# Kernel tuning notes

Measured on AMD Instinct MI355X. Metric: run time of the kernel, lower is better.

## Reference

```python
import jax, jax.numpy as jnp
import numpy as np

VOCAB = 50000
D = 300          # w2v vector_size
B = 2048         # sentences
L = 64           # maxlen
S = 2048         # total seeds (= sum of num_clusters[0])
C = 64           # clusters
LS = 8           # maxlen_seed
ANPHA = 0.5


def setup_inputs() -> dict:
    key = jax.random.key(0)
    ks = jax.random.split(key, 4)
    return {
        "sents": jax.random.randint(ks[0], (B, L), 0, VOCAB),
        "seeds": jax.random.randint(ks[1], (S, LS), 0, VOCAB),
        "num_clusters": jnp.full((1, C), S // C, dtype=jnp.int32),
        "num_arr": 0,
        "mask": jnp.ones((B, L), jnp.float32),
        "flag": 1,
        "emb_teacher": jax.random.normal(ks[2], (VOCAB, D), jnp.float32) * 0.1,
        "emb_student": jax.random.normal(ks[3], (VOCAB, D), jnp.float32) * 0.1,
    }


def _sent_emb(tok_emb, mask):
    # masked mean pooling over tokens: tok_emb [B,L,D], mask [B,L]
    denom = jnp.clip(mask.sum(-1, keepdims=True), 1.0)
    return (tok_emb * mask[..., None]).sum(1) / denom


def _seed_emb(tok_emb):
    # plain mean pooling over seed-phrase tokens: [S,LS,D] -> [S,D]
    return tok_emb.mean(1)


def _segment_max_arg(pro, lens):
    # pro [B,S]; lens [C] segment lengths summing to S (ragged segments along axis 1)
    Ssz = pro.shape[1]
    Csz = lens.shape[0]
    csum = jnp.cumsum(lens)
    starts = csum - lens
    seg = jnp.searchsorted(csum, jnp.arange(Ssz), side="right")   # [S] segment ids
    m = jax.ops.segment_max(pro.T, seg, num_segments=Csz)          # [C,B] per-segment max
    is_max = pro.T == m[seg]                                       # [S,B]
    local = jnp.arange(Ssz) - starts[seg]                          # index within segment
    arg = jax.ops.segment_min(jnp.where(is_max, local[:, None], Ssz), seg,
                              num_segments=Csz)                    # first argmax (torch tie rule)
    return m.T, arg.T                                              # [B,C], [B,C]


def _normalize(x):
    # Normalize(): class-probabilities + reliability (confidence vs uniform)
    p = jax.nn.softmax(x, axis=-1)
    reli = jnp.max(p, axis=-1, keepdims=True) - 1.0 / x.shape[-1]
    return p, reli


def reference(sents, seeds, num_clusters, num_arr, mask, flag,
              emb_teacher, emb_student):
    lens = num_clusters[0]

    # teacher branch
    snt_t = _sent_emb(emb_teacher[sents], mask)        # [B,D]
    sd_t = _seed_emb(emb_teacher[seeds])               # [S,D]
    pro_t = jnp.einsum("bd,sd->bs", snt_t, sd_t)       # [B,S]

    # student branch
    snt_s = _sent_emb(emb_student[sents], mask)
    sd_s = _seed_emb(emb_student[seeds])
    pro_s = jnp.einsum("bd,sd->bs", snt_s, sd_s)

    # ragged per-cluster max / argmax (replaces the torch loop + cat)
    pro_s_max, index_max = _segment_max_arg(pro_s, lens)   # [B,C]
    pro_t_max, _ = _segment_max_arg(pro_t, lens)           # [B,C]

    predict_t, reli_t = _normalize(pro_t_max)

    if flag:  # flag is a static python int -> loss branch
        denta = predict_t - pro_s_max
        loss = ((1.0 + ANPHA * jnp.abs(reli_t)) * denta * denta).sum()
        return loss / predict_t.shape[0]
    else:
        return jnp.argmax(pro_s_max, axis=-1)
```

## Files before the change

kernel.cpp:

```cpp
#include <hip/hip_runtime.h>
#include <hip/hip_bf16.h>

#define BB 2048
#define LL 64
#define SS 2048
#define LSEED 8
#define CC 64
#define DD 300
#define NC4 75
#define KP 320

typedef __attribute__((ext_vector_type(8))) short short8;
typedef __attribute__((ext_vector_type(4))) float f32x4;

__device__ __forceinline__ unsigned enc_f(float f) {
    unsigned u = __float_as_uint(f);
    return (u & 0x80000000u) ? ~u : (u | 0x80000000u);
}
__device__ __forceinline__ float dec_f(unsigned k) {
    unsigned u = (k & 0x80000000u) ? (k ^ 0x80000000u) : ~k;
    return __uint_as_float(u);
}
__device__ __forceinline__ unsigned short f2bf(float f) {
    unsigned u = __float_as_uint(f);
    u += 0x7fffu + ((u >> 16) & 1u);
    return (unsigned short)(u >> 16);
}
__device__ __forceinline__ void gload_lds16(const void* g, void* l) {
    __builtin_amdgcn_global_load_lds(
        (const __attribute__((address_space(1))) void*)g,
        (__attribute__((address_space(3))) void*)l, 16, 0, 0);
}

__global__ __launch_bounds__(256) void pool_kernel(
    const int* __restrict__ sents, const int* __restrict__ seeds,
    const int* __restrict__ lens, const float* __restrict__ mask,
    const float* __restrict__ emb_t, const float* __restrict__ emb_s,
    unsigned short* __restrict__ snt_t, unsigned short* __restrict__ snt_s,
    unsigned short* __restrict__ sd_t, unsigned short* __restrict__ sd_s,
    unsigned* __restrict__ keys_all, int* __restrict__ seg,
    float* __restrict__ out0) {
    const int bid = blockIdx.x, tid = threadIdx.x;

    if (tid < 64) keys_all[bid * 64 + tid] = 0u;
    if (bid == 0) {
        if (tid == 0) *out0 = 0.f;
        for (int i = tid * 8; i < tid * 8 + 8; i++) {
            int c = 0, cum = lens[0];
            while (i >= cum && c < CC - 1) { c++; cum += lens[c]; }
            seg[i] = c;
        }
    }

    __shared__ float4 pt[3 * NC4];
    __shared__ float4 ps[3 * NC4];
    __shared__ int toks[LL];
    __shared__ float msk[LL];
    __shared__ float denom_sh;

    const int g = tid / NC4;
    const int c = tid - g * NC4;

    if (bid < BB) {
        const int b = bid;
        if (tid < LL) {
            float v = mask[b * LL + tid];
            msk[tid] = v;
            toks[tid] = sents[b * LL + tid];
#pragma unroll
            for (int d = 32; d; d >>= 1) v += __shfl_xor(v, d);
            if (tid == 0) denom_sh = fmaxf(v, 1.0f);
        }
        __syncthreads();
        if (g < 3) {
            float4 at = {0.f, 0.f, 0.f, 0.f}, as = {0.f, 0.f, 0.f, 0.f};
#pragma unroll 4
            for (int l = g; l < LL; l += 3) {
                size_t o = (size_t)toks[l] * DD;
                float m = msk[l];
                float4 vt = *(const float4*)(emb_t + o + 4 * c);
                float4 vs = *(const float4*)(emb_s + o + 4 * c);
                at.x = fmaf(m, vt.x, at.x); at.y = fmaf(m, vt.y, at.y);
                at.z = fmaf(m, vt.z, at.z); at.w = fmaf(m, vt.w, at.w);
                as.x = fmaf(m, vs.x, as.x); as.y = fmaf(m, vs.y, as.y);
                as.z = fmaf(m, vs.z, as.z); as.w = fmaf(m, vs.w, as.w);
            }
            pt[g * NC4 + c] = at;
            ps[g * NC4 + c] = as;
        }
        __syncthreads();
        float scale = 1.0f / denom_sh;
        if (tid < 150) {
            int table = tid / NC4, cc = tid - table * NC4;
            const float4* P = table ? ps : pt;
            float4 a = P[cc], b2 = P[NC4 + cc], d2 = P[2 * NC4 + cc];
            ushort4 o;
            o.x = f2bf((a.x + b2.x + d2.x) * scale);
            o.y = f2bf((a.y + b2.y + d2.y) * scale);
            o.z = f2bf((a.z + b2.z + d2.z) * scale);
            o.w = f2bf((a.w + b2.w + d2.w) * scale);
            unsigned short* dst = (table ? snt_s : snt_t) + (size_t)b * KP + 4 * cc;
            *(ushort4*)dst = o;
        } else if (tid >= 160 && tid < 170) {
            int k = tid - 160;
            unsigned short* dst = ((k < 5) ? snt_t : snt_s) + (size_t)b * KP + 300 + 4 * (k % 5);
            *(ushort4*)dst = (ushort4){0, 0, 0, 0};
        }
    } else {
        const int s = bid - BB;
        if (tid < LSEED) toks[tid] = seeds[s * LSEED + tid];
        __syncthreads();
        if (g < 3) {
            float4 at = {0.f, 0.f, 0.f, 0.f}, as = {0.f, 0.f, 0.f, 0.f};
#pragma unroll
            for (int l = g; l < LSEED; l += 3) {
                size_t o = (size_t)toks[l] * DD;
                float4 vt = *(const float4*)(emb_t + o + 4 * c);
                float4 vs = *(const float4*)(emb_s + o + 4 * c);
                at.x += vt.x; at.y += vt.y; at.z += vt.z; at.w += vt.w;
                as.x += vs.x; as.y += vs.y; as.z += vs.z; as.w += vs.w;
            }
            pt[g * NC4 + c] = at;
            ps[g * NC4 + c] = as;
        }
        __syncthreads();
        const float scale = 1.0f / LSEED;
        if (tid < 150) {
            int table = tid / NC4, cc = tid - table * NC4;
            const float4* P = table ? ps : pt;
            float4 a = P[cc], b2 = P[NC4 + cc], d2 = P[2 * NC4 + cc];
            ushort4 o;
            o.x = f2bf((a.x + b2.x + d2.x) * scale);
            o.y = f2bf((a.y + b2.y + d2.y) * scale);
            o.z = f2bf((a.z + b2.z + d2.z) * scale);
            o.w = f2bf((a.w + b2.w + d2.w) * scale);
            unsigned short* dst = (table ? sd_s : sd_t) + (size_t)s * KP + 4 * cc;
            *(ushort4*)dst = o;
        } else if (tid >= 160 && tid < 170) {
            int k = tid - 160;
            unsigned short* dst = ((k < 5) ? sd_t : sd_s) + (size_t)s * KP + 300 + 4 * (k % 5);
            *(ushort4*)dst = (ushort4){0, 0, 0, 0};
        }
    }
}

__global__ __launch_bounds__(256) void gemm_max_kernel(
    const unsigned short* __restrict__ snt_t, const unsigned short* __restrict__ snt_s,
    const unsigned short* __restrict__ sd_t, const unsigned short* __restrict__ sd_s,
    const int* __restrict__ seg,
    unsigned* __restrict__ keys_t, unsigned* __restrict__ keys_s) {
    const int branch = blockIdx.z;
    const unsigned short* Ag = branch ? snt_s : snt_t;
    const unsigned short* Bg = branch ? sd_s : sd_t;
    unsigned* keys = branch ? keys_s : keys_t;

    const int tid = threadIdx.x;
    const int wave = tid >> 6, lane = tid & 63;
    const int quad = lane >> 4, l16 = lane & 15;
    const int wm = wave >> 1, wn = wave & 1;
    const int row0 = blockIdx.y * 128, col0 = blockIdx.x * 128;

    __shared__ __align__(16) char smem[33792 + 512];
    unsigned short* As = (unsigned short*)smem;
    unsigned short* Bs = As + 128 * 32;
    float* Dl = (float*)smem;
    int* segs = (int*)(smem + 33792);

    if (tid < 128) segs[tid] = seg[col0 + tid];

    const int lr = lane >> 2, lp = lane & 3;

    f32x4 acc[4][4];
#pragma unroll
    for (int i = 0; i < 4; i++)
#pragma unroll
        for (int j = 0; j < 4; j++) acc[i][j] = (f32x4)0.f;

#pragma unroll 1
    for (int kt = 0; kt < KP / 32; kt++) {
        const int k0 = kt * 32;
        __syncthreads();
#pragma unroll
        for (int i = 0; i < 2; i++) {
            int rb = wave * 32 + i * 16;
            gload_lds16(Ag + (size_t)(row0 + rb + lr) * KP + k0 + lp * 8,
                        As + rb * 32);
            gload_lds16(Bg + (size_t)(col0 + rb + lr) * KP + k0 + lp * 8,
                        Bs + rb * 32);
        }
        __syncthreads();
        short8 af[4], bfr[4];
#pragma unroll
        for (int mt = 0; mt < 4; mt++)
            af[mt] = *(const short8*)(As + (wm * 64 + mt * 16 + l16) * 32 + quad * 8);
#pragma unroll
        for (int nt = 0; nt < 4; nt++)
            bfr[nt] = *(const short8*)(Bs + (wn * 64 + nt * 16 + l16) * 32 + quad * 8);
#pragma unroll
        for (int mt = 0; mt < 4; mt++)
#pragma unroll
            for (int nt = 0; nt < 4; nt++)
                acc[mt][nt] = __builtin_amdgcn_mfma_f32_16x16x32_bf16(
                    af[mt], bfr[nt], acc[mt][nt], 0, 0, 0);
    }

#pragma unroll 1
    for (int h = 0; h < 2; h++) {
        __syncthreads();
        if (wn == h) {
#pragma unroll
            for (int mt = 0; mt < 4; mt++)
#pragma unroll
                for (int nt = 0; nt < 4; nt++)
#pragma unroll
                    for (int reg = 0; reg < 4; reg++)
                        Dl[(wm * 64 + mt * 16 + quad * 4 + reg) * 66 + nt * 16 + l16] =
                            acc[mt][nt][reg];
        }
        __syncthreads();
        int r = tid >> 1, j0 = (tid & 1) * 32;
        float cur = Dl[r * 66 + j0];
        int cs = segs[h * 64 + j0];
#pragma unroll
        for (int j = 1; j < 32; j++) {
            int sgj = segs[h * 64 + j0 + j];
            float v = Dl[r * 66 + j0 + j];
            if (sgj == cs) {
                cur = fmaxf(cur, v);
            } else {
                atomicMax(&keys[(size_t)(row0 + r) * CC + cs], enc_f(cur));
                cs = sgj;
                cur = v;
            }
        }
        atomicMax(&keys[(size_t)(row0 + r) * CC + cs], enc_f(cur));
    }
}

__global__ __launch_bounds__(256) void loss_kernel(
    const unsigned* __restrict__ keys_t, const unsigned* __restrict__ keys_s,
    float* __restrict__ out) {
    int tid = threadIdx.x, w = tid >> 6, lane = tid & 63;
    int row = blockIdx.x * 4 + w;
    float t = dec_f(keys_t[row * CC + lane]);
    float s = dec_f(keys_s[row * CC + lane]);
    float m = t;
#pragma unroll
    for (int d = 32; d; d >>= 1) m = fmaxf(m, __shfl_xor(m, d));
    float e = expf(t - m);
    float sum = e;
#pragma unroll
    for (int d = 32; d; d >>= 1) sum += __shfl_xor(sum, d);
    float p = e / sum;
    float reli = 1.0f / sum - (1.0f / CC);
    float denta = p - s;
    float term = (1.0f + 0.5f * fabsf(reli)) * denta * denta;
#pragma unroll
    for (int d = 32; d; d >>= 1) term += __shfl_xor(term, d);
    __shared__ float blk[4];
    if (lane == 0) blk[w] = term;
    __syncthreads();
    if (tid == 0)
        atomicAdd(out, (blk[0] + blk[1] + blk[2] + blk[3]) * (1.0f / BB));
}

extern "C" void kernel_launch(void* const* d_in, const int* in_sizes, int n_in,
                              void* d_out, int out_size, void* d_ws, size_t ws_size,
                              hipStream_t stream) {
    const int*   sents = (const int*)d_in[0];
    const int*   seeds = (const int*)d_in[1];
    const int*   lens  = (const int*)d_in[2];
    const float* mask  = (const float*)d_in[4];
    const float* emb_t = (const float*)d_in[6];
    const float* emb_s = (const float*)d_in[7];
    float* out = (float*)d_out;

    char* w = (char*)d_ws;
    unsigned short* snt_t = (unsigned short*)w; w += (size_t)BB * KP * 2;
    unsigned short* snt_s = (unsigned short*)w; w += (size_t)BB * KP * 2;
    unsigned short* sd_t  = (unsigned short*)w; w += (size_t)SS * KP * 2;
    unsigned short* sd_s  = (unsigned short*)w; w += (size_t)SS * KP * 2;
    unsigned* keys_t = (unsigned*)w; w += (size_t)BB * CC * 4;
    unsigned* keys_s = (unsigned*)w; w += (size_t)BB * CC * 4;
    int* seg = (int*)w;              w += (size_t)SS * 4;

    pool_kernel<<<BB + SS, 256, 0, stream>>>(sents, seeds, lens, mask, emb_t, emb_s,
                                             snt_t, snt_s, sd_t, sd_s,
                                             keys_t, seg, out);
    gemm_max_kernel<<<dim3(SS / 128, BB / 128, 2), 256, 0, stream>>>(
        snt_t, snt_s, sd_t, sd_s, seg, keys_t, keys_s);
    loss_kernel<<<BB / 4, 256, 0, stream>>>(keys_t, keys_s, out);
}
```

Measured before the change: 197.4 us.

## Double-buffer GEMM LDS tiles and fuse loss into GEMM via last-block counter

```diff
diff --git a/kernel.cpp b/kernel.cpp
--- a/kernel.cpp
+++ b/kernel.cpp
@@ -39,12 +39,13 @@
     unsigned short* __restrict__ snt_t, unsigned short* __restrict__ snt_s,
     unsigned short* __restrict__ sd_t, unsigned short* __restrict__ sd_s,
     unsigned* __restrict__ keys_all, int* __restrict__ seg,
-    float* __restrict__ out0) {
+    unsigned* __restrict__ cnt, float* __restrict__ out0) {
     const int bid = blockIdx.x, tid = threadIdx.x;
 
     if (tid < 64) keys_all[bid * 64 + tid] = 0u;
     if (bid == 0) {
         if (tid == 0) *out0 = 0.f;
+        if (tid < 16) cnt[tid] = 0u;
         for (int i = tid * 8; i < tid * 8 + 8; i++) {
             int c = 0, cum = lens[0];
             while (i >= cum && c < CC - 1) { c++; cum += lens[c]; }
@@ -148,7 +149,8 @@
     const unsigned short* __restrict__ snt_t, const unsigned short* __restrict__ snt_s,
     const unsigned short* __restrict__ sd_t, const unsigned short* __restrict__ sd_s,
     const int* __restrict__ seg,
-    unsigned* __restrict__ keys_t, unsigned* __restrict__ keys_s) {
+    unsigned* __restrict__ keys_t, unsigned* __restrict__ keys_s,
+    unsigned* __restrict__ cnt, float* __restrict__ out) {
     const int branch = blockIdx.z;
     const unsigned short* Ag = branch ? snt_s : snt_t;
     const unsigned short* Bg = branch ? sd_s : sd_t;
@@ -161,10 +163,10 @@
     const int row0 = blockIdx.y * 128, col0 = blockIdx.x * 128;
 
     __shared__ __align__(16) char smem[33792 + 512];
-    unsigned short* As = (unsigned short*)smem;
-    unsigned short* Bs = As + 128 * 32;
+    unsigned short* Sb = (unsigned short*)smem;
     float* Dl = (float*)smem;
     int* segs = (int*)(smem + 33792);
+    __shared__ unsigned last_sh;
 
     if (tid < 128) segs[tid] = seg[col0 + tid];
 
@@ -176,19 +178,25 @@
 #pragma unroll
         for (int j = 0; j < 4; j++) acc[i][j] = (f32x4)0.f;
 
+    auto stage = [&](int kt) {
+        const int b = kt & 1, k0 = kt * 32;
+        unsigned short* As = Sb + b * 8192;
+        unsigned short* Bs = As + 4096;
+#pragma unroll
+        for (int i = 0; i < 2; i++) {
+            int rb = wave * 32 + i * 16;
+            gload_lds16(Ag + (size_t)(row0 + rb + lr) * KP + k0 + lp * 8, As + rb * 32);
+            gload_lds16(Bg + (size_t)(col0 + rb + lr) * KP + k0 + lp * 8, Bs + rb * 32);
+        }
+    };
+
+    stage(0);
 #pragma unroll 1
     for (int kt = 0; kt < KP / 32; kt++) {
-        const int k0 = kt * 32;
-        __syncthreads();
-#pragma unroll
-        for (int i = 0; i < 2; i++) {
-            int rb = wave * 32 + i * 16;
-            gload_lds16(Ag + (size_t)(row0 + rb + lr) * KP + k0 + lp * 8,
-                        As + rb * 32);
-            gload_lds16(Bg + (size_t)(col0 + rb + lr) * KP + k0 + lp * 8,
-                        Bs + rb * 32);
-        }
-        __syncthreads();
+        __syncthreads();
+        if (kt < KP / 32 - 1) stage(kt + 1);
+        const unsigned short* As = Sb + (kt & 1) * 8192;
+        const unsigned short* Bs = As + 4096;
         short8 af[4], bfr[4];
 #pragma unroll
         for (int mt = 0; mt < 4; mt++)
@@ -235,33 +243,40 @@
         }
         atomicMax(&keys[(size_t)(row0 + r) * CC + cs], enc_f(cur));
     }
-}
-
-__global__ __launch_bounds__(256) void loss_kernel(
-    const unsigned* __restrict__ keys_t, const unsigned* __restrict__ keys_s,
-    float* __restrict__ out) {
-    int tid = threadIdx.x, w = tid >> 6, lane = tid & 63;
-    int row = blockIdx.x * 4 + w;
-    float t = dec_f(keys_t[row * CC + lane]);
-    float s = dec_f(keys_s[row * CC + lane]);
-    float m = t;
-#pragma unroll
-    for (int d = 32; d; d >>= 1) m = fmaxf(m, __shfl_xor(m, d));
-    float e = expf(t - m);
-    float sum = e;
-#pragma unroll
-    for (int d = 32; d; d >>= 1) sum += __shfl_xor(sum, d);
-    float p = e / sum;
-    float reli = 1.0f / sum - (1.0f / CC);
-    float denta = p - s;
-    float term = (1.0f + 0.5f * fabsf(reli)) * denta * denta;
-#pragma unroll
-    for (int d = 32; d; d >>= 1) term += __shfl_xor(term, d);
-    __shared__ float blk[4];
-    if (lane == 0) blk[w] = term;
+
     __syncthreads();
-    if (tid == 0)
-        atomicAdd(out, (blk[0] + blk[1] + blk[2] + blk[3]) * (1.0f / BB));
+    if (tid == 0) {
+        __threadfence();
+        last_sh = atomicAdd(&cnt[blockIdx.y], 1u);
+    }
+    __syncthreads();
+    if (last_sh == 31u) {
+        __threadfence();
+        float part = 0.f;
+#pragma unroll 1
+        for (int it = 0; it < 32; it++) {
+            size_t row = (size_t)blockIdx.y * 128 + it * 4 + wave;
+            float t = dec_f(__hip_atomic_load(&keys_t[row * CC + lane],
+                                              __ATOMIC_RELAXED, __HIP_MEMORY_SCOPE_AGENT));
+            float s = dec_f(__hip_atomic_load(&keys_s[row * CC + lane],
+                                              __ATOMIC_RELAXED, __HIP_MEMORY_SCOPE_AGENT));
+            float m = t;
+#pragma unroll
+            for (int d = 32; d; d >>= 1) m = fmaxf(m, __shfl_xor(m, d));
+            float e = expf(t - m);
+            float sum = e;
+#pragma unroll
+            for (int d = 32; d; d >>= 1) sum += __shfl_xor(sum, d);
+            float p = e / sum;
+            float reli = 1.0f / sum - (1.0f / CC);
+            float denta = p - s;
+            float term = (1.0f + 0.5f * fabsf(reli)) * denta * denta;
+#pragma unroll
+            for (int d = 32; d; d >>= 1) term += __shfl_xor(term, d);
+            part += term;
+        }
+        if (lane == 0) atomicAdd(out, part * (1.0f / BB));
+    }
 }
 
 extern "C" void kernel_launch(void* const* d_in, const int* in_sizes, int n_in,
@@ -283,11 +298,11 @@
     unsigned* keys_t = (unsigned*)w; w += (size_t)BB * CC * 4;
     unsigned* keys_s = (unsigned*)w; w += (size_t)BB * CC * 4;
     int* seg = (int*)w;              w += (size_t)SS * 4;
+    unsigned* cnt = (unsigned*)w;    w += 16 * 4;
 
     pool_kernel<<<BB + SS, 256, 0, stream>>>(sents, seeds, lens, mask, emb_t, emb_s,
                                              snt_t, snt_s, sd_t, sd_s,
-                                             keys_t, seg, out);
+                                             keys_t, seg, cnt, out);
     gemm_max_kernel<<<dim3(SS / 128, BB / 128, 2), 256, 0, stream>>>(
-        snt_t, snt_s, sd_t, sd_s, seg, keys_t, keys_s);
-    loss_kernel<<<BB / 4, 256, 0, stream>>>(keys_t, keys_s, out);
-}
+        snt_t, snt_s, sd_t, sd_s, seg, keys_t, keys_s, cnt, out);
+}
```

Result: slower. 228.8 us (+15.9%).
